# Kernel optimization log

Hardware: AMD Instinct MI355X
Metric: run time of the kernel (lower is better)

## Reference

```python
import jax, jax.numpy as jnp
import numpy as np

EMBED, HEADS, LEVELS, POINTS = 256, 8, 4, 4
SPATIAL_SHAPES = np.array([[128, 128], [64, 64], [32, 32], [16, 16]], dtype=np.int32)


def _grid_init_bias():
    # Faithful reproduction of the sampling_offsets bias init (per-head directional grid).
    thetas = np.arange(HEADS, dtype=np.float32) * (2.0 * np.pi / HEADS)
    g = np.stack([np.cos(thetas), np.sin(thetas)], -1)
    g = g / np.abs(g).max(-1, keepdims=True)
    g = np.tile(g.reshape(HEADS, 1, 1, 2), (1, LEVELS, POINTS, 1))
    for i in range(POINTS):
        g[:, :, i, :] *= i + 1
    return g.reshape(-1).astype(np.float32)


def setup_inputs() -> dict:
    key = jax.random.key(0)
    ks = jax.random.split(key, 8)
    bs = 2
    V = int((SPATIAL_SHAPES[:, 0] * SPATIAL_SHAPES[:, 1]).sum())  # 21760
    Q = V  # encoder self-attention
    C = EMBED
    n_off = HEADS * LEVELS * POINTS * 2
    n_attn = HEADS * LEVELS * POINTS
    inv_sqrt_c = 1.0 / np.sqrt(C)
    return {
        "query": jax.random.normal(ks[0], (bs, Q, C), jnp.float32),
        "value": jax.random.normal(ks[1], (bs, V, C), jnp.float32),
        "reference_points": jax.random.uniform(ks[2], (bs, Q, LEVELS, 2), jnp.float32),
        "spatial_shapes": SPATIAL_SHAPES,  # static int array
        # learned parameters (torch Linear stored as [in, out]: y = x @ W + b)
        "W_off": jax.random.normal(ks[3], (C, n_off), jnp.float32) * 0.01,
        "b_off": jnp.asarray(_grid_init_bias()),
        "W_attn": jax.random.normal(ks[4], (C, n_attn), jnp.float32) * 0.02,
        "b_attn": jnp.zeros((n_attn,), jnp.float32),
        "W_v": jax.random.normal(ks[5], (C, C), jnp.float32) * inv_sqrt_c,
        "b_v": jnp.zeros((C,), jnp.float32),
        "W_out": jax.random.normal(ks[6], (C, C), jnp.float32) * inv_sqrt_c,
        "b_out": jnp.zeros((C,), jnp.float32),
    }


def _ms_deform_attn(query, value, reference_points, shapes,
                    W_off, b_off, W_attn, b_attn, W_v, b_v, W_out, b_out):
    bs, Q, C = query.shape
    d = C // HEADS
    # value projection -> [bs, heads, V, d]
    val = (value @ W_v + b_v).reshape(bs, -1, HEADS, d).transpose(0, 2, 1, 3)
    # sampling offsets and attention weights from query
    off = (query @ W_off + b_off).reshape(bs, Q, HEADS, LEVELS, POINTS, 2)
    attn = jax.nn.softmax(
        (query @ W_attn + b_attn).reshape(bs, Q, HEADS, LEVELS * POINTS), axis=-1
    ).reshape(bs, Q, HEADS, LEVELS, POINTS)
    # offset normalizer is (W, H) per level
    norm = jnp.asarray(np.stack([shapes[:, 1], shapes[:, 0]], -1), jnp.float32)  # [L,2]
    loc = reference_points[:, :, None, :, None, :] + off / norm[None, None, None, :, None, :]

    out = jnp.zeros((bs, HEADS, Q, d), query.dtype)
    start = 0
    for l in range(LEVELS):
        H, W = int(shapes[l, 0]), int(shapes[l, 1])
        v_l = val[:, :, start:start + H * W]  # [bs, heads, H*W, d]
        start += H * W
        loc_l = loc[:, :, :, l]    # [bs, Q, heads, P, 2] in [0,1]
        attn_l = attn[:, :, :, l]  # [bs, Q, heads, P]
        # grid_sample(align_corners=False, padding_mode='zeros') semantics
        g = 2.0 * loc_l - 1.0
        x = (g[..., 0] + 1.0) * 0.5 * W - 0.5
        y = (g[..., 1] + 1.0) * 0.5 * H - 0.5
        x0 = jnp.floor(x)
        y0 = jnp.floor(y)
        for dx in (0, 1):
            for dy in (0, 1):
                xi = x0 + dx
                yi = y0 + dy
                w = (1.0 - jnp.abs(x - xi)) * (1.0 - jnp.abs(y - yi))
                valid = (xi >= 0) & (xi <= W - 1) & (yi >= 0) & (yi <= H - 1)
                w = jnp.where(valid, w, 0.0) * attn_l  # fused corner + attention weight
                idx = (jnp.clip(yi, 0, H - 1).astype(jnp.int32) * W
                       + jnp.clip(xi, 0, W - 1).astype(jnp.int32))  # [bs,Q,heads,P]
                idx_t = jnp.transpose(idx, (0, 2, 1, 3)).reshape(bs, HEADS, Q * POINTS)
                vals = jnp.take_along_axis(v_l, idx_t[..., None], axis=2)
                vals = vals.reshape(bs, HEADS, Q, POINTS, d)
                out = out + jnp.einsum('bhqpd,bqhp->bhqd', vals, w)
    out = out.transpose(0, 2, 1, 3).reshape(bs, Q, C)  # heads-major channel layout
    return out @ W_out + b_out


def reference(query, value, reference_points, spatial_shapes,
              W_off, b_off, W_attn, b_attn, W_v, b_v, W_out, b_out):
    shapes = np.asarray(spatial_shapes)  # static
    return _ms_deform_attn(query, value, reference_points, shapes,
                           W_off, b_off, W_attn, b_attn, W_v, b_v, W_out, b_out)
```

## Files before the change

kernel.cpp:

```cpp
#include <hip/hip_runtime.h>
#include <math.h>

#define QN 21760
#define MTOT 43520
#define SZBQC 11141120

typedef __attribute__((ext_vector_type(8))) short bf16x8;
typedef __attribute__((ext_vector_type(4))) float f32x4;

__device__ inline ushort f2bf(float f) {
  union { float f; uint u; } v; v.f = f;
  return (ushort)((v.u + 0x7FFFu + ((v.u >> 16) & 1u)) >> 16);
}
__device__ inline uint pk2(float lo, float hi) { return (uint)f2bf(lo) | ((uint)f2bf(hi) << 16); }

__device__ inline void g2l(const ushort* g, ushort* l) {
  __builtin_amdgcn_global_load_lds(
      (const __attribute__((address_space(1))) void*)g,
      (__attribute__((address_space(3))) void*)l, 16, 0, 0);
}

__global__ __launch_bounds__(256) void prep_weights(
    const float* __restrict__ Wv, const float* __restrict__ Wout,
    const float* __restrict__ Woff, const float* __restrict__ Wattn,
    const float* __restrict__ boff, const float* __restrict__ battn,
    ushort* __restrict__ wv_t, ushort* __restrict__ wout_t,
    ushort* __restrict__ wol_t, float* __restrict__ biasf) {
  int bidx = blockIdx.x, t = threadIdx.x;
  if (bidx < 256) {
    int idx = bidx * 256 + t; int n = idx >> 8, k = idx & 255;
    wv_t[idx] = f2bf(Wv[(size_t)k * 256 + n]);
  } else if (bidx < 512) {
    int idx = (bidx - 256) * 256 + t; int n = idx >> 8, k = idx & 255;
    wout_t[idx] = f2bf(Wout[(size_t)k * 256 + n]);
  } else {
    int idx = (bidx - 512) * 256 + t; int n = idx >> 8, k = idx & 255;
    float v = (n < 256) ? Woff[(size_t)k * 256 + n] : Wattn[(size_t)k * 128 + (n - 256)];
    wol_t[idx] = f2bf(v);
    if (idx < 384) biasf[idx] = (idx < 256) ? boff[idx] : battn[idx - 256];
  }
}


__global__ __launch_bounds__(256) void gemm_in(
    const float* __restrict__ value, const float* __restrict__ query,
    const ushort* __restrict__ Wv, const ushort* __restrict__ Wol,
    const float* __restrict__ bv, const float* __restrict__ bol,
    ushort* __restrict__ val_out, float* __restrict__ offlog) {
  __shared__ ushort As[2][4096];
  __shared__ ushort Bs[2][4096];
  const int t = threadIdx.x, wave = t >> 6, lane = t & 63;
  const int bx = blockIdx.y, bm = blockIdx.x * 128;
  const bool isVal = bx < 2;
  const float* A   = isVal ? value : query;
  const ushort* Bt = isVal ? (Wv + (size_t)bx * 128 * 256)
                           : (Wol + (size_t)(bx - 2) * 128 * 256);
  const int wm = (wave >> 1) * 64, wn = (wave & 1) * 64;
  const int l15 = lane & 15, l4 = lane >> 4;
  const int pc = l4 ^ ((l15 >> 1) & 3);

  const int srow = lane >> 2;
  const int sch  = (lane & 3) ^ ((lane >> 3) & 3);
  const ushort* Bg = Bt + (size_t)(32 * wave + srow) * 256 + sch * 8;
  ushort* lb[2] = { &Bs[0][(32 * wave) * 32], &Bs[1][(32 * wave) * 32] };

  f32x4 acc[4][4];
#pragma unroll
  for (int i = 0; i < 4; ++i)
#pragma unroll
    for (int j = 0; j < 4; ++j) acc[i][j] = (f32x4){0.f, 0.f, 0.f, 0.f};

  int arow[4], apart[4];
#pragma unroll
  for (int i = 0; i < 4; ++i) {
    int c = t + i * 256; arow[i] = c >> 3; apart[i] = c & 7;
  }

  {
    float4 pa[4];
#pragma unroll
    for (int i = 0; i < 4; ++i)
      pa[i] = *(const float4*)&A[(size_t)(bm + arow[i]) * 256 + apart[i] * 4];
    g2l(Bg, lb[0]); g2l(Bg + 16 * 256, lb[0] + 16 * 32);
#pragma unroll
    for (int i = 0; i < 4; ++i) {
      int pc16 = (apart[i] >> 1) ^ ((arow[i] >> 1) & 3);
      ushort4 hv = { f2bf(pa[i].x), f2bf(pa[i].y), f2bf(pa[i].z), f2bf(pa[i].w) };
      *(ushort4*)&As[0][arow[i] * 32 + pc16 * 8 + (apart[i] & 1) * 4] = hv;
    }
  }

  for (int k = 0; k < 8; ++k) {
    __syncthreads();
    const int cur = k & 1, nxt = cur ^ 1;
    float4 pa[4];
    if (k < 7) {
      int k1 = (k + 1) * 32;
#pragma unroll
      for (int i = 0; i < 4; ++i)
        pa[i] = *(const float4*)&A[(size_t)(bm + arow[i]) * 256 + k1 + apart[i] * 4];
      g2l(Bg + k1, lb[nxt]); g2l(Bg + 16 * 256 + k1, lb[nxt] + 16 * 32);
    }
    bf16x8 af[4], bfr[4];
#pragma unroll
    for (int mi = 0; mi < 4; ++mi)
      af[mi] = *(const bf16x8*)&As[cur][(wm + mi * 16 + l15) * 32 + pc * 8];
#pragma unroll
    for (int ni = 0; ni < 4; ++ni)
      bfr[ni] = *(const bf16x8*)&Bs[cur][(wn + ni * 16 + l15) * 32 + pc * 8];
#pragma unroll
    for (int mi = 0; mi < 4; ++mi)
#pragma unroll
      for (int ni = 0; ni < 4; ++ni)
        acc[mi][ni] = __builtin_amdgcn_mfma_f32_16x16x32_bf16(af[mi], bfr[ni], acc[mi][ni], 0, 0, 0);
    if (k < 7) {
#pragma unroll
      for (int i = 0; i < 4; ++i) {
        int pc16 = (apart[i] >> 1) ^ ((arow[i] >> 1) & 3);
        ushort4 hv = { f2bf(pa[i].x), f2bf(pa[i].y), f2bf(pa[i].z), f2bf(pa[i].w) };
        *(ushort4*)&As[nxt][arow[i] * 32 + pc16 * 8 + (apart[i] & 1) * 4] = hv;
      }
    }
  }

  if (isVal) {
    _Float16* vo = (_Float16*)val_out;
#pragma unroll
    for (int mi = 0; mi < 4; ++mi)
#pragma unroll
      for (int ni = 0; ni < 4; ++ni) {
        int col = bx * 128 + wn + ni * 16 + l15;
        float bb = bv[col];
        int hh = col >> 5, c = col & 31;
#pragma unroll
        for (int r = 0; r < 4; ++r) {
          int row = bm + wm + mi * 16 + l4 * 4 + r;
          int b = (row >= QN) ? 1 : 0;
          int vpos = row - b * QN;
          vo[((size_t)(b * 8 + hh) * QN + vpos) * 32 + c] = (_Float16)(acc[mi][ni][r] + bb);
        }
      }
  } else {
#pragma unroll
    for (int mi = 0; mi < 4; ++mi)
#pragma unroll
      for (int ni = 0; ni < 4; ++ni) {
        int col = (bx - 2) * 128 + wn + ni * 16 + l15;
        float bb = bol[col];
#pragma unroll
        for (int r = 0; r < 4; ++r) {
          int row = bm + wm + mi * 16 + l4 * 4 + r;
          offlog[(size_t)row * 384 + col] = acc[mi][ni][r] + bb;
        }
      }
  }
}

__global__ __launch_bounds__(256) void gemm_out(
    const ushort* __restrict__ A, const ushort* __restrict__ Bt,
    const float* __restrict__ bias, float* __restrict__ C) {
  __shared__ ushort As[2][4096];
  __shared__ ushort Bs[2][4096];
  const int t = threadIdx.x, wave = t >> 6, lane = t & 63;
  const int bm = blockIdx.x * 128, bn = blockIdx.y * 128;
  const int wm = (wave >> 1) * 64, wn = (wave & 1) * 64;
  const int l15 = lane & 15, l4 = lane >> 4;
  const int pc = l4 ^ ((l15 >> 1) & 3);

  const int srow = lane >> 2;
  const int sch  = (lane & 3) ^ ((lane >> 3) & 3);
  const ushort* Ag = A + (size_t)(bm + 32 * wave + srow) * 256 + sch * 8;
  const ushort* Bg = Bt + (size_t)(bn + 32 * wave + srow) * 256 + sch * 8;
  ushort* la[2] = { &As[0][(32 * wave) * 32], &As[1][(32 * wave) * 32] };
  ushort* lb[2] = { &Bs[0][(32 * wave) * 32], &Bs[1][(32 * wave) * 32] };

  f32x4 acc[4][4];
#pragma unroll
  for (int i = 0; i < 4; ++i)
#pragma unroll
    for (int j = 0; j < 4; ++j) acc[i][j] = (f32x4){0.f, 0.f, 0.f, 0.f};

  g2l(Ag, la[0]); g2l(Ag + 16 * 256, la[0] + 16 * 32);
  g2l(Bg, lb[0]); g2l(Bg + 16 * 256, lb[0] + 16 * 32);

  for (int k = 0; k < 8; ++k) {
    __syncthreads();
    const int cur = k & 1, nxt = cur ^ 1;
    if (k < 7) {
      int k1 = (k + 1) * 32;
      g2l(Ag + k1, la[nxt]); g2l(Ag + 16 * 256 + k1, la[nxt] + 16 * 32);
      g2l(Bg + k1, lb[nxt]); g2l(Bg + 16 * 256 + k1, lb[nxt] + 16 * 32);
    }
    bf16x8 af[4], bfr[4];
#pragma unroll
    for (int mi = 0; mi < 4; ++mi)
      af[mi] = *(const bf16x8*)&As[cur][(wm + mi * 16 + l15) * 32 + pc * 8];
#pragma unroll
    for (int ni = 0; ni < 4; ++ni)
      bfr[ni] = *(const bf16x8*)&Bs[cur][(wn + ni * 16 + l15) * 32 + pc * 8];
#pragma unroll
    for (int mi = 0; mi < 4; ++mi)
#pragma unroll
      for (int ni = 0; ni < 4; ++ni)
        acc[mi][ni] = __builtin_amdgcn_mfma_f32_16x16x32_bf16(af[mi], bfr[ni], acc[mi][ni], 0, 0, 0);
  }

#pragma unroll
  for (int mi = 0; mi < 4; ++mi)
#pragma unroll
    for (int ni = 0; ni < 4; ++ni) {
      int col = bn + wn + ni * 16 + l15;
      float bb = bias[col];
#pragma unroll
      for (int r = 0; r < 4; ++r) {
        int row = bm + wm + mi * 16 + l4 * 4 + r;
        C[(size_t)row * 256 + col] = acc[mi][ni][r] + bb;
      }
    }
}

__device__ inline void fmah(float* a, uint4 u, float wv) {
  union { uint4 u; _Float16 h[8]; } c; c.u = u;
#pragma unroll
  for (int i = 0; i < 8; ++i) a[i] = fmaf((float)c.h[i], wv, a[i]);
}

__global__ __launch_bounds__(256) void msda_sample(
    const ushort* __restrict__ val, const float* __restrict__ offlog,
    const float* __restrict__ ref, ushort* __restrict__ interm) {
  const int lsz[4]    = {128, 64, 32, 16};
  const int lstart[4] = {0, 16384, 20480, 21504};

  int h   = blockIdx.x & 7;
  int z   = blockIdx.x >> 3;
  int sub = threadIdx.x & 3;
  int bq  = z * 64 + (threadIdx.x >> 2);
  int b   = (bq >= QN) ? 1 : 0;

  const float* lgp = offlog + (size_t)bq * 384 + 256 + h * 16;
  float w[16];
  {
    float4 a0 = *(const float4*)(lgp);
    float4 a1 = *(const float4*)(lgp + 4);
    float4 a2 = *(const float4*)(lgp + 8);
    float4 a3 = *(const float4*)(lgp + 12);
    w[0]=a0.x; w[1]=a0.y; w[2]=a0.z; w[3]=a0.w;
    w[4]=a1.x; w[5]=a1.y; w[6]=a1.z; w[7]=a1.w;
    w[8]=a2.x; w[9]=a2.y; w[10]=a2.z; w[11]=a2.w;
    w[12]=a3.x; w[13]=a3.y; w[14]=a3.z; w[15]=a3.w;
  }
  float m = -1e30f;
#pragma unroll
  for (int s = 0; s < 16; ++s) m = fmaxf(m, w[s]);
  float sum = 0.f;
#pragma unroll
  for (int s = 0; s < 16; ++s) { w[s] = __expf(w[s] - m); sum += w[s]; }
  float inv = __builtin_amdgcn_rcpf(sum);

  const float* offp = offlog + (size_t)bq * 384 + h * 32;
  const float* refp = ref + (size_t)bq * 8;
  const ushort* vb  = val + ((size_t)(b * 8 + h) * QN) * 32 + sub * 8;

  float acc[8];
#pragma unroll
  for (int i = 0; i < 8; ++i) acc[i] = 0.f;

#pragma unroll
  for (int l = 0; l < 4; ++l) {
    float4 o0 = *(const float4*)(offp + l * 8);
    float4 o1 = *(const float4*)(offp + l * 8 + 4);
    float ox[4] = { o0.x, o0.z, o1.x, o1.z };
    float oy[4] = { o0.y, o0.w, o1.y, o1.w };
    const int   W = lsz[l];
    const float fW = (float)W;
    const int   base = lstart[l];
    const float rx = refp[l * 2 + 0], ry = refp[l * 2 + 1];
    const float xb = rx * fW - 0.5f;
    const float yb = ry * fW - 0.5f;
#pragma unroll
    for (int p = 0; p < 4; ++p) {
      float x = xb + ox[p];
      float y = yb + oy[p];
      float x0f = floorf(x), y0f = floorf(y);
      int   x0 = (int)x0f,   y0 = (int)y0f;
      float fx = x - x0f,    fy = y - y0f;
      float a = w[l * 4 + p] * inv;
      float wx0  = ((unsigned)x0       < (unsigned)W) ? (1.f - fx) : 0.f;
      float wx1  = ((unsigned)(x0 + 1) < (unsigned)W) ? fx         : 0.f;
      float wy0a = (((unsigned)y0       < (unsigned)W) ? (1.f - fy) : 0.f) * a;
      float wy1a = (((unsigned)(y0 + 1) < (unsigned)W) ? fy         : 0.f) * a;
      int xc0 = min(max(x0, 0), W - 1);
      int xc1 = min(max(x0 + 1, 0), W - 1);
      int yc0 = min(max(y0, 0), W - 1);
      int yc1 = min(max(y0 + 1, 0), W - 1);
      int row0 = base + yc0 * W;
      int row1 = base + yc1 * W;
      const ushort* p00 = vb + (size_t)(row0 + xc0) * 32;
      const ushort* p10 = vb + (size_t)(row0 + xc1) * 32;
      const ushort* p01 = vb + (size_t)(row1 + xc0) * 32;
      const ushort* p11 = vb + (size_t)(row1 + xc1) * 32;
      uint4 u00 = *(const uint4*)p00;
      uint4 u10 = *(const uint4*)p10;
      uint4 u01 = *(const uint4*)p01;
      uint4 u11 = *(const uint4*)p11;
      fmah(acc, u00, wx0 * wy0a);
      fmah(acc, u10, wx1 * wy0a);
      fmah(acc, u01, wx0 * wy1a);
      fmah(acc, u11, wx1 * wy1a);
    }
  }

  uint4 o;
  o.x = pk2(acc[0], acc[1]); o.y = pk2(acc[2], acc[3]);
  o.z = pk2(acc[4], acc[5]); o.w = pk2(acc[6], acc[7]);
  *(uint4*)(interm + (size_t)bq * 256 + h * 32 + sub * 8) = o;
}

extern "C" void kernel_launch(void* const* d_in, const int* in_sizes, int n_in,
                              void* d_out, int out_size, void* d_ws, size_t ws_size,
                              hipStream_t stream) {
  const float* query = (const float*)d_in[0];
  const float* value = (const float*)d_in[1];
  const float* ref   = (const float*)d_in[2];
  const float* W_off  = (const float*)d_in[4];
  const float* b_off  = (const float*)d_in[5];
  const float* W_attn = (const float*)d_in[6];
  const float* b_attn = (const float*)d_in[7];
  const float* W_v    = (const float*)d_in[8];
  const float* b_v    = (const float*)d_in[9];
  const float* W_out  = (const float*)d_in[10];
  const float* b_out  = (const float*)d_in[11];
  float* out = (float*)d_out;

  char* wsb = (char*)d_ws;
  ushort* ws_wv     = (ushort*)(wsb + 0);
  ushort* ws_wol    = (ushort*)(wsb + 131072);
  ushort* ws_wout   = (ushort*)(wsb + 327680);
  float*  ws_biasf  = (float*)(wsb + 458752);
  ushort* ws_val    = (ushort*)(wsb + 462848);
  ushort* ws_interm = (ushort*)(wsb + 22745088);
  float*  ws_offlog = (float*)(wsb + 45027328);
  size_t need = (size_t)45027328 + 66846720;
  if (ws_size < need) return;

  dim3 blk(256);
  prep_weights<<<dim3(896), blk, 0, stream>>>(W_v, W_out, W_off, W_attn, b_off, b_attn,
                                              ws_wv, ws_wout, ws_wol, ws_biasf);
  gemm_in<<<dim3(340, 5), blk, 0, stream>>>(value, query, ws_wv, ws_wol, b_v, ws_biasf,
                                            ws_val, ws_offlog);
  msda_sample<<<dim3(5440), blk, 0, stream>>>(ws_val, ws_offlog, ref, ws_interm);
  gemm_out<<<dim3(340, 2), blk, 0, stream>>>(ws_interm, ws_wout, b_out, out);
}
```

Baseline: 286.4 us.

## Split per-level sampling math across lanes and swizzle GEMM block order

The sampling kernel now has each of the 4 lanes serving a query-head compute softmax, coordinates, bilinear weights and addresses for one level. The results are then broadcast with shuffles, so the four lanes no longer repeat the same scalar work, at the cost of 7 shuffles per sample point. Both GEMMs use a 1D grid remapped so 8 consecutive row-tiles are grouped across all column-tiles, aiming at better L2 reuse of A rows. This adds a few idle padded blocks.

After: 277.3 us. 3.2% less time.

```diff
diff --git a/kernel.cpp b/kernel.cpp
--- a/kernel.cpp
+++ b/kernel.cpp
@@ -49,8 +49,13 @@
     ushort* __restrict__ val_out, float* __restrict__ offlog) {
   __shared__ ushort As[2][4096];
   __shared__ ushort Bs[2][4096];
+  const int bid = blockIdx.x;
+  const int q5  = bid >> 3;
+  const int bxv = (bid & 7) + 8 * (q5 / 5);
+  const int bx  = q5 % 5;
+  if (bxv >= 340) return;
   const int t = threadIdx.x, wave = t >> 6, lane = t & 63;
-  const int bx = blockIdx.y, bm = blockIdx.x * 128;
+  const int bm = bxv * 128;
   const bool isVal = bx < 2;
   const float* A   = isVal ? value : query;
   const ushort* Bt = isVal ? (Wv + (size_t)bx * 128 * 256)
@@ -161,8 +166,13 @@
     const float* __restrict__ bias, float* __restrict__ C) {
   __shared__ ushort As[2][4096];
   __shared__ ushort Bs[2][4096];
+  const int bid = blockIdx.x;
+  const int q2  = bid >> 3;
+  const int bxv = (bid & 7) + 8 * (q2 >> 1);
+  const int byv = q2 & 1;
+  if (bxv >= 340) return;
   const int t = threadIdx.x, wave = t >> 6, lane = t & 63;
-  const int bm = blockIdx.x * 128, bn = blockIdx.y * 128;
+  const int bm = bxv * 128, bn = byv * 128;
   const int wm = (wave >> 1) * 64, wn = (wave & 1) * 64;
   const int l15 = lane & 15, l4 = lane >> 4;
   const int pc = l4 ^ ((l15 >> 1) & 3);
@@ -228,85 +238,87 @@
 __global__ __launch_bounds__(256) void msda_sample(
     const ushort* __restrict__ val, const float* __restrict__ offlog,
     const float* __restrict__ ref, ushort* __restrict__ interm) {
-  const int lsz[4]    = {128, 64, 32, 16};
-  const int lstart[4] = {0, 16384, 20480, 21504};
-
   int h   = blockIdx.x & 7;
   int z   = blockIdx.x >> 3;
   int sub = threadIdx.x & 3;
   int bq  = z * 64 + (threadIdx.x >> 2);
   int b   = (bq >= QN) ? 1 : 0;
+  const uint sub8 = (uint)(sub * 8);
+  const ushort* vb = val + (size_t)((uint)(b * 8 + h) * (uint)QN) * 32u + sub8;
 
   const float* lgp = offlog + (size_t)bq * 384 + 256 + h * 16;
-  float w[16];
-  {
-    float4 a0 = *(const float4*)(lgp);
-    float4 a1 = *(const float4*)(lgp + 4);
-    float4 a2 = *(const float4*)(lgp + 8);
-    float4 a3 = *(const float4*)(lgp + 12);
-    w[0]=a0.x; w[1]=a0.y; w[2]=a0.z; w[3]=a0.w;
-    w[4]=a1.x; w[5]=a1.y; w[6]=a1.z; w[7]=a1.w;
-    w[8]=a2.x; w[9]=a2.y; w[10]=a2.z; w[11]=a2.w;
-    w[12]=a3.x; w[13]=a3.y; w[14]=a3.z; w[15]=a3.w;
-  }
-  float m = -1e30f;
-#pragma unroll
-  for (int s = 0; s < 16; ++s) m = fmaxf(m, w[s]);
-  float sum = 0.f;
-#pragma unroll
-  for (int s = 0; s < 16; ++s) { w[s] = __expf(w[s] - m); sum += w[s]; }
-  float inv = __builtin_amdgcn_rcpf(sum);
-
+  float4 lg = *(const float4*)(lgp + sub * 4);
+  float m = fmaxf(fmaxf(lg.x, lg.y), fmaxf(lg.z, lg.w));
+  m = fmaxf(m, __shfl_xor(m, 1, 64));
+  m = fmaxf(m, __shfl_xor(m, 2, 64));
+  float e0 = __expf(lg.x - m), e1 = __expf(lg.y - m),
+        e2 = __expf(lg.z - m), e3 = __expf(lg.w - m);
+  float s = e0 + e1 + e2 + e3;
+  s += __shfl_xor(s, 1, 64);
+  s += __shfl_xor(s, 2, 64);
+  float inv = __builtin_amdgcn_rcpf(s);
+  float aw[4] = { e0 * inv, e1 * inv, e2 * inv, e3 * inv };
+
+  const int  Wl  = 128 >> sub;
+  const uint t16 = 65536u >> (sub + sub);
+  const int  lst = (int)((65536u - t16) / 3u);
+  const float fW = (float)Wl;
   const float* offp = offlog + (size_t)bq * 384 + h * 32;
-  const float* refp = ref + (size_t)bq * 8;
-  const ushort* vb  = val + ((size_t)(b * 8 + h) * QN) * 32 + sub * 8;
+  float4 o0 = *(const float4*)(offp + sub * 8);
+  float4 o1 = *(const float4*)(offp + sub * 8 + 4);
+  float2 rf = *(const float2*)(ref + (size_t)bq * 8 + sub * 2);
+  const float xb = rf.x * fW - 0.5f;
+  const float yb = rf.y * fW - 0.5f;
+  float ox[4] = { o0.x, o0.z, o1.x, o1.z };
+  float oy[4] = { o0.y, o0.w, o1.y, o1.w };
+
+  uint  pA0[4], pA1[4], pDX[4];
+  float pX0[4], pX1[4], pY0[4], pY1[4];
+#pragma unroll
+  for (int p = 0; p < 4; ++p) {
+    float x = xb + ox[p], y = yb + oy[p];
+    float x0f = floorf(x), y0f = floorf(y);
+    float fx = x - x0f, fy = y - y0f;
+    int x0 = (int)x0f, y0 = (int)y0f;
+    float a = aw[p];
+    pX0[p] = ((uint)x0       < (uint)Wl) ? (1.f - fx) : 0.f;
+    pX1[p] = ((uint)(x0 + 1) < (uint)Wl) ? fx         : 0.f;
+    pY0[p] = (((uint)y0       < (uint)Wl) ? (1.f - fy) : 0.f) * a;
+    pY1[p] = (((uint)(y0 + 1) < (uint)Wl) ? fy         : 0.f) * a;
+    int xc0 = min(max(x0, 0), Wl - 1);
+    int xc1 = min(max(x0 + 1, 0), Wl - 1);
+    int yc0 = min(max(y0, 0), Wl - 1);
+    int yc1 = min(max(y0 + 1, 0), Wl - 1);
+    pA0[p] = (uint)((lst + yc0 * Wl + xc0) * 32);
+    pA1[p] = (uint)((lst + yc1 * Wl + xc0) * 32);
+    pDX[p] = (uint)((xc1 - xc0) * 32);
+  }
 
   float acc[8];
 #pragma unroll
   for (int i = 0; i < 8; ++i) acc[i] = 0.f;
 
+  const int lanebase = (threadIdx.x & 63) & 60;
 #pragma unroll
   for (int l = 0; l < 4; ++l) {
-    float4 o0 = *(const float4*)(offp + l * 8);
-    float4 o1 = *(const float4*)(offp + l * 8 + 4);
-    float ox[4] = { o0.x, o0.z, o1.x, o1.z };
-    float oy[4] = { o0.y, o0.w, o1.y, o1.w };
-    const int   W = lsz[l];
-    const float fW = (float)W;
-    const int   base = lstart[l];
-    const float rx = refp[l * 2 + 0], ry = refp[l * 2 + 1];
-    const float xb = rx * fW - 0.5f;
-    const float yb = ry * fW - 0.5f;
+    const int src = lanebase | l;
 #pragma unroll
     for (int p = 0; p < 4; ++p) {
-      float x = xb + ox[p];
-      float y = yb + oy[p];
-      float x0f = floorf(x), y0f = floorf(y);
-      int   x0 = (int)x0f,   y0 = (int)y0f;
-      float fx = x - x0f,    fy = y - y0f;
-      float a = w[l * 4 + p] * inv;
-      float wx0  = ((unsigned)x0       < (unsigned)W) ? (1.f - fx) : 0.f;
-      float wx1  = ((unsigned)(x0 + 1) < (unsigned)W) ? fx         : 0.f;
-      float wy0a = (((unsigned)y0       < (unsigned)W) ? (1.f - fy) : 0.f) * a;
-      float wy1a = (((unsigned)(y0 + 1) < (unsigned)W) ? fy         : 0.f) * a;
-      int xc0 = min(max(x0, 0), W - 1);
-      int xc1 = min(max(x0 + 1, 0), W - 1);
-      int yc0 = min(max(y0, 0), W - 1);
-      int yc1 = min(max(y0 + 1, 0), W - 1);
-      int row0 = base + yc0 * W;
-      int row1 = base + yc1 * W;
-      const ushort* p00 = vb + (size_t)(row0 + xc0) * 32;
-      const ushort* p10 = vb + (size_t)(row0 + xc1) * 32;
-      const ushort* p01 = vb + (size_t)(row1 + xc0) * 32;
-      const ushort* p11 = vb + (size_t)(row1 + xc1) * 32;
-      uint4 u00 = *(const uint4*)p00;
-      uint4 u10 = *(const uint4*)p10;
-      uint4 u01 = *(const uint4*)p01;
-      uint4 u11 = *(const uint4*)p11;
-      fmah(acc, u00, wx0 * wy0a);
-      fmah(acc, u10, wx1 * wy0a);
-      fmah(acc, u01, wx0 * wy1a);
-      fmah(acc, u11, wx1 * wy1a);
+      uint  A0  = (uint)__shfl((int)pA0[p], src, 64);
+      uint  A1  = (uint)__shfl((int)pA1[p], src, 64);
+      uint  DX  = (uint)__shfl((int)pDX[p], src, 64);
+      float wx0 = __shfl(pX0[p], src, 64);
+      float wx1 = __shfl(pX1[p], src, 64);
+      float wy0 = __shfl(pY0[p], src, 64);
+      float wy1 = __shfl(pY1[p], src, 64);
+      uint4 u00 = *(const uint4*)(vb + A0);
+      uint4 u01 = *(const uint4*)(vb + A0 + DX);
+      uint4 u10 = *(const uint4*)(vb + A1);
+      uint4 u11 = *(const uint4*)(vb + A1 + DX);
+      fmah(acc, u00, wx0 * wy0);
+      fmah(acc, u01, wx1 * wy0);
+      fmah(acc, u10, wx0 * wy1);
+      fmah(acc, u11, wx1 * wy1);
     }
   }
 
@@ -346,8 +358,8 @@
   dim3 blk(256);
   prep_weights<<<dim3(896), blk, 0, stream>>>(W_v, W_out, W_off, W_attn, b_off, b_attn,
                                               ws_wv, ws_wout, ws_wol, ws_biasf);
-  gemm_in<<<dim3(340, 5), blk, 0, stream>>>(value, query, ws_wv, ws_wol, b_v, ws_biasf,
-                                            ws_val, ws_offlog);
+  gemm_in<<<dim3(1720), blk, 0, stream>>>(value, query, ws_wv, ws_wol, b_v, ws_biasf,
+                                          ws_val, ws_offlog);
   msda_sample<<<dim3(5440), blk, 0, stream>>>(ws_val, ws_offlog, ref, ws_interm);
-  gemm_out<<<dim3(340, 2), blk, 0, stream>>>(ws_interm, ws_wout, b_out, out);
-}
+  gemm_out<<<dim3(688), blk, 0, stream>>>(ws_interm, ws_wout, b_out, out);
+}
```
